# Optimization experiments

Measured on AMD Instinct MI355X. Metric: run time of the kernel, lower is better.

## Reference

```python
import jax, jax.numpy as jnp
import numpy as np

B, NQ, NK, D, H = 4, 512, 512, 128, 32  # batch, n_queries, n_keys, kq_size, mlp hidden


def setup_inputs() -> dict:
    key = jax.random.key(0)
    ks = jax.random.split(key, 7)
    s_in = 1.0 / np.sqrt(2 * D)
    s_h = 1.0 / np.sqrt(H)
    return {
        "keys": jax.random.normal(ks[0], (B, NK, D), dtype=jnp.float32),
        "queries": jax.random.normal(ks[1], (B, NQ, D), dtype=jnp.float32),
        # first MLP layer Linear(2D, H) split into key-half and query-half
        "Wk": jax.random.uniform(ks[2], (D, H), jnp.float32, -s_in, s_in),
        "Wq": jax.random.uniform(ks[3], (D, H), jnp.float32, -s_in, s_in),
        "b1": jax.random.uniform(ks[4], (H,), jnp.float32, -s_in, s_in),
        # second MLP layer Linear(H, 1)
        "w2": jax.random.uniform(ks[5], (H,), jnp.float32, -s_h, s_h),
        "b2": jax.random.uniform(ks[6], (), jnp.float32, -s_h, s_h),
    }


def reference(keys, queries, Wk, Wq, b1, w2, b2):
    # AdditiveScorer: logits[b,q,k] = w2 . tanh(W1 @ [keys[b,k]; queries[b,q]] + b1) + b2
    # Split the concat-linear into two GEMMs (identical math, no [B,Q,K,2D] tensor).
    kh = jnp.einsum("bkd,dh->bkh", keys, Wk)            # (B, NK, H)
    qh = jnp.einsum("bqd,dh->bqh", queries, Wq)          # (B, NQ, H)
    h = jnp.tanh(qh[:, :, None, :] + kh[:, None, :, :] + b1)  # (B, NQ, NK, H)
    logits = jnp.einsum("bqkh,h->bqk", h, w2) + b2       # (B, NQ, NK)
    attn = jax.nn.softmax(logits, axis=-1)               # softmax over keys
    context = jnp.einsum("bqk,bkd->bqd", attn, keys)     # weighted value sum (values = keys)
    return context
```

## Files before the change

### kernel.cpp

```cpp
#include <hip/hip_runtime.h>

#define B 4
#define NQ 512
#define NK 512
#define D 128
#define H 32
#define G 4
#define PS 2.8853900817779268f

__device__ __forceinline__ float rcp_f(float x)  { return __builtin_amdgcn_rcpf(x); }
__device__ __forceinline__ float exp2_f(float x) { return __builtin_amdgcn_exp2f(x); }

__device__ __forceinline__ void fma4(float4& a, const float4& v, float s) {
    a.x = fmaf(s, v.x, a.x);
    a.y = fmaf(s, v.y, a.y);
    a.z = fmaf(s, v.z, a.z);
    a.w = fmaf(s, v.w, a.w);
}

__global__ __launch_bounds__(256) void proj_kernel(
    const float* __restrict__ keys, const float* __restrict__ queries,
    const float* __restrict__ Wk, const float* __restrict__ Wq,
    const float* __restrict__ b1,
    float* __restrict__ Ek, float* __restrict__ eq)
{
    __shared__ float xs[8][D];
    const int tid = threadIdx.x;
    const int r0 = blockIdx.x * 8;
    const bool is_q = (r0 >= B * NK);
    const float* __restrict__ X = is_q ? (queries + (size_t)(r0 - B * NK) * D)
                                       : (keys + (size_t)r0 * D);
    const float* __restrict__ W = is_q ? Wq : Wk;

    reinterpret_cast<float4*>(&xs[0][0])[tid] =
        reinterpret_cast<const float4*>(X)[tid];
    __syncthreads();

    const int lr = tid >> 5;
    const int h  = tid & 31;
    float a0 = 0.f, a1 = 0.f, a2 = 0.f, a3 = 0.f;
    const float4* x4 = reinterpret_cast<const float4*>(&xs[lr][0]);
    #pragma unroll
    for (int i = 0; i < D / 4; ++i) {
        float4 v = x4[i];
        a0 = fmaf(v.x, W[(4 * i + 0) * H + h], a0);
        a1 = fmaf(v.y, W[(4 * i + 1) * H + h], a1);
        a2 = fmaf(v.z, W[(4 * i + 2) * H + h], a2);
        a3 = fmaf(v.w, W[(4 * i + 3) * H + h], a3);
    }
    float acc = (a0 + a1) + (a2 + a3);
    if (is_q) {
        const int rq = r0 - B * NK + lr;
        eq[(size_t)rq * H + h] = exp2_f(acc * PS);
    } else {
        const int r = r0 + lr;
        const int b = r >> 9;
        const int k = r & (NK - 1);
        Ek[((size_t)b * H + h) * NK + k] = exp2_f((acc + b1[h]) * PS);
    }
}

__global__ __launch_bounds__(512, 4) void attend_kernel(
    const float* __restrict__ keys,
    const float* __restrict__ Ek,
    const float* __restrict__ eq,
    const float* __restrict__ w2,
    float* __restrict__ outp)
{
    __shared__ float exw[NK][G];
    __shared__ float accm[16][G][D];
    float* red = &accm[0][0][0];

    const int tid = threadIdx.x;
    const int b   = blockIdx.x >> 7;
    const int q0  = (blockIdx.x & 127) * G;

    const float* Ekc = Ek + (size_t)b * H * NK + tid;
    float ek[H];
    #pragma unroll
    for (int h = 0; h < H; ++h) ek[h] = Ekc[h * NK];

    const float* eqb = eq + ((size_t)b * NQ + q0) * H;
    float acc[G];
    #pragma unroll
    for (int g = 0; g < G; ++g) acc[g] = 0.f;

    #pragma unroll
    for (int h4 = 0; h4 < H; h4 += 4) {
        const float w0 = w2[h4 + 0];
        const float w1 = w2[h4 + 1];
        const float wc = w2[h4 + 2];
        const float w3 = w2[h4 + 3];
        #pragma unroll
        for (int g = 0; g < G; ++g) {
            const float d0 = fmaf(eqb[g * H + h4 + 0], ek[h4 + 0], 1.f);
            const float d1 = fmaf(eqb[g * H + h4 + 1], ek[h4 + 1], 1.f);
            const float d2 = fmaf(eqb[g * H + h4 + 2], ek[h4 + 2], 1.f);
            const float d3 = fmaf(eqb[g * H + h4 + 3], ek[h4 + 3], 1.f);
            const float nab = fmaf(w1, d0, w0 * d1);
            const float ncd = fmaf(w3, d2, wc * d3);
            const float dab = d0 * d1;
            const float dcd = d2 * d3;
            const float n4  = fmaf(nab, dcd, ncd * dab);
            const float d4  = dab * dcd;
            acc[g] = fmaf(n4, rcp_f(d4), acc[g]);
        }
    }
    float e0 = exp2_f(-PS * acc[0]);
    float e1 = exp2_f(-PS * acc[1]);
    float e2 = exp2_f(-PS * acc[2]);
    float e3 = exp2_f(-PS * acc[3]);

    float s0 = e0, s1 = e1, s2 = e2, s3 = e3;
    #pragma unroll
    for (int off = 32; off; off >>= 1) {
        s0 += __shfl_xor(s0, off);
        s1 += __shfl_xor(s1, off);
        s2 += __shfl_xor(s2, off);
        s3 += __shfl_xor(s3, off);
    }
    if ((tid & 63) == 0)
        *reinterpret_cast<float4*>(red + (tid >> 6) * G) = float4{s0, s1, s2, s3};
    __syncthreads();
    float4 sum = {0.f, 0.f, 0.f, 0.f};
    #pragma unroll
    for (int p = 0; p < 8; ++p) {
        const float4 v = *reinterpret_cast<const float4*>(red + p * G);
        sum.x += v.x; sum.y += v.y; sum.z += v.z; sum.w += v.w;
    }
    *reinterpret_cast<float4*>(&exw[tid][0]) =
        float4{e0 * rcp_f(sum.x), e1 * rcp_f(sum.y),
               e2 * rcp_f(sum.z), e3 * rcp_f(sum.w)};
    __syncthreads();

    const int dg = tid & 31;
    const int kp = tid >> 5;
    const float4* k4 = reinterpret_cast<const float4*>(
        keys + ((size_t)b * NK + kp * 32) * D) + dg;
    float4 a0 = {0,0,0,0}, a1 = a0, a2 = a0, a3 = a0;

    float4 kbA[8], kbB[8];
    #pragma unroll
    for (int j = 0; j < 8; ++j) kbA[j] = k4[(size_t)j * (D / 4)];
    #pragma unroll
    for (int c = 0; c < 4; ++c) {
        float4* cur = (c & 1) ? kbB : kbA;
        float4* nxt = (c & 1) ? kbA : kbB;
        if (c < 3) {
            #pragma unroll
            for (int j = 0; j < 8; ++j)
                nxt[j] = k4[(size_t)((c + 1) * 8 + j) * (D / 4)];
        }
        #pragma unroll
        for (int j = 0; j < 8; ++j) {
            const int kk = c * 8 + j;
            const float4 ev = *reinterpret_cast<const float4*>(&exw[kp * 32 + kk][0]);
            fma4(a0, cur[j], ev.x);
            fma4(a1, cur[j], ev.y);
            fma4(a2, cur[j], ev.z);
            fma4(a3, cur[j], ev.w);
        }
    }
    *reinterpret_cast<float4*>(&accm[kp][0][4 * dg]) = a0;
    *reinterpret_cast<float4*>(&accm[kp][1][4 * dg]) = a1;
    *reinterpret_cast<float4*>(&accm[kp][2][4 * dg]) = a2;
    *reinterpret_cast<float4*>(&accm[kp][3][4 * dg]) = a3;
    __syncthreads();

    const int g = tid >> 7;
    const int d = tid & 127;
    float r = 0.f;
    #pragma unroll
    for (int p = 0; p < 16; ++p) r += accm[p][g][d];
    outp[((size_t)b * NQ + q0 + g) * D + d] = r;
}

extern "C" void kernel_launch(void* const* d_in, const int* in_sizes, int n_in,
                              void* d_out, int out_size, void* d_ws, size_t ws_size,
                              hipStream_t stream) {
    const float* keys    = (const float*)d_in[0];
    const float* queries = (const float*)d_in[1];
    const float* Wk      = (const float*)d_in[2];
    const float* Wq      = (const float*)d_in[3];
    const float* b1      = (const float*)d_in[4];
    const float* w2      = (const float*)d_in[5];
    float* out = (float*)d_out;

    float* Ek = (float*)d_ws;
    float* eq = Ek + (size_t)B * H * NK;

    const int proj_blocks = (B * NK + B * NQ) / 8;
    proj_kernel<<<proj_blocks, 256, 0, stream>>>(keys, queries, Wk, Wq, b1, Ek, eq);
    attend_kernel<<<B * NQ / G, 512, 0, stream>>>(keys, Ek, eq, w2, out);
}
```

Baseline: 20.10 us.

## Compute attention-weighted key sum with split-bf16 MFMA instead of fp32 FMAs

The proj kernel now also writes the keys transposed as high/low bf16 pairs. The attend kernel stores the softmax weights as hi/lo bf16 in shared memory and computes the context with three 16x16x32 bf16 MFMAs per k-step, which approximates fp32 precision. This drops the fp32 FMA loop and the 16-way shared-memory partial reduction. The cost is extra workspace traffic, bf16 split work, and a small precision loss from dropping the lo*lo term. Only a quarter of the lanes write output, since the MFMA result is replicated across them.

Result: slower. 30.92 us (+53.8%).

```diff
diff --git a/kernel.cpp b/kernel.cpp
--- a/kernel.cpp
+++ b/kernel.cpp
@@ -7,22 +7,27 @@
 #define H 32
 #define G 4
 #define PS 2.8853900817779268f
+#define NKP (NK + 8)
+
+typedef float f32x4 __attribute__((ext_vector_type(4)));
+typedef short bf16x8 __attribute__((ext_vector_type(8)));
 
 __device__ __forceinline__ float rcp_f(float x)  { return __builtin_amdgcn_rcpf(x); }
 __device__ __forceinline__ float exp2_f(float x) { return __builtin_amdgcn_exp2f(x); }
 
-__device__ __forceinline__ void fma4(float4& a, const float4& v, float s) {
-    a.x = fmaf(s, v.x, a.x);
-    a.y = fmaf(s, v.y, a.y);
-    a.z = fmaf(s, v.z, a.z);
-    a.w = fmaf(s, v.w, a.w);
+__device__ __forceinline__ void bf16_split(float x, unsigned short& h, unsigned short& l) {
+    unsigned bits = __float_as_uint(x);
+    h = (unsigned short)(bits >> 16);
+    float hf = __uint_as_float((unsigned)h << 16);
+    l = (unsigned short)(__float_as_uint(x - hf) >> 16);
 }
 
 __global__ __launch_bounds__(256) void proj_kernel(
     const float* __restrict__ keys, const float* __restrict__ queries,
     const float* __restrict__ Wk, const float* __restrict__ Wq,
     const float* __restrict__ b1,
-    float* __restrict__ Ek, float* __restrict__ eq)
+    float* __restrict__ Ek, float* __restrict__ eq,
+    unsigned short* __restrict__ khi, unsigned short* __restrict__ klo)
 {
     __shared__ float xs[8][D];
     const int tid = threadIdx.x;
@@ -58,18 +63,34 @@
         const int k = r & (NK - 1);
         Ek[((size_t)b * H + h) * NK + k] = exp2_f((acc + b1[h]) * PS);
     }
+
+    if (!is_q) {
+        const int bb = r0 >> 9;
+        const int k0 = r0 & (NK - 1);
+        const int d  = tid >> 1;
+        const int kq = (tid & 1) * 4;
+        ushort4 h4, l4;
+        unsigned short* hp = reinterpret_cast<unsigned short*>(&h4);
+        unsigned short* lp = reinterpret_cast<unsigned short*>(&l4);
+        #pragma unroll
+        for (int j = 0; j < 4; ++j)
+            bf16_split(xs[kq + j][d], hp[j], lp[j]);
+        *reinterpret_cast<ushort4*>(&khi[((size_t)bb * D + d) * NK + k0 + kq]) = h4;
+        *reinterpret_cast<ushort4*>(&klo[((size_t)bb * D + d) * NK + k0 + kq]) = l4;
+    }
 }
 
 __global__ __launch_bounds__(512, 4) void attend_kernel(
-    const float* __restrict__ keys,
+    const unsigned short* __restrict__ khi,
+    const unsigned short* __restrict__ klo,
     const float* __restrict__ Ek,
     const float* __restrict__ eq,
     const float* __restrict__ w2,
     float* __restrict__ outp)
 {
-    __shared__ float exw[NK][G];
-    __shared__ float accm[16][G][D];
-    float* red = &accm[0][0][0];
+    __shared__ unsigned short ex_hi[G][NKP];
+    __shared__ unsigned short ex_lo[G][NKP];
+    __shared__ float red[8][G];
 
     const int tid = threadIdx.x;
     const int b   = blockIdx.x >> 7;
@@ -102,8 +123,7 @@
             const float dab = d0 * d1;
             const float dcd = d2 * d3;
             const float n4  = fmaf(nab, dcd, ncd * dab);
-            const float d4  = dab * dcd;
-            acc[g] = fmaf(n4, rcp_f(d4), acc[g]);
+            acc[g] = fmaf(n4, rcp_f(dab * dcd), acc[g]);
         }
     }
     float e0 = exp2_f(-PS * acc[0]);
@@ -120,59 +140,51 @@
         s3 += __shfl_xor(s3, off);
     }
     if ((tid & 63) == 0)
-        *reinterpret_cast<float4*>(red + (tid >> 6) * G) = float4{s0, s1, s2, s3};
+        *reinterpret_cast<float4*>(&red[tid >> 6][0]) = float4{s0, s1, s2, s3};
     __syncthreads();
     float4 sum = {0.f, 0.f, 0.f, 0.f};
     #pragma unroll
     for (int p = 0; p < 8; ++p) {
-        const float4 v = *reinterpret_cast<const float4*>(red + p * G);
+        const float4 v = *reinterpret_cast<const float4*>(&red[p][0]);
         sum.x += v.x; sum.y += v.y; sum.z += v.z; sum.w += v.w;
     }
-    *reinterpret_cast<float4*>(&exw[tid][0]) =
-        float4{e0 * rcp_f(sum.x), e1 * rcp_f(sum.y),
-               e2 * rcp_f(sum.z), e3 * rcp_f(sum.w)};
+    {
+        const float v0 = e0 * rcp_f(sum.x);
+        const float v1 = e1 * rcp_f(sum.y);
+        const float v2 = e2 * rcp_f(sum.z);
+        const float v3 = e3 * rcp_f(sum.w);
+        unsigned short h, l;
+        bf16_split(v0, h, l); ex_hi[0][tid] = h; ex_lo[0][tid] = l;
+        bf16_split(v1, h, l); ex_hi[1][tid] = h; ex_lo[1][tid] = l;
+        bf16_split(v2, h, l); ex_hi[2][tid] = h; ex_lo[2][tid] = l;
+        bf16_split(v3, h, l); ex_hi[3][tid] = h; ex_lo[3][tid] = l;
+    }
     __syncthreads();
 
-    const int dg = tid & 31;
-    const int kp = tid >> 5;
-    const float4* k4 = reinterpret_cast<const float4*>(
-        keys + ((size_t)b * NK + kp * 32) * D) + dg;
-    float4 a0 = {0,0,0,0}, a1 = a0, a2 = a0, a3 = a0;
-
-    float4 kbA[8], kbB[8];
-    #pragma unroll
-    for (int j = 0; j < 8; ++j) kbA[j] = k4[(size_t)j * (D / 4)];
-    #pragma unroll
-    for (int c = 0; c < 4; ++c) {
-        float4* cur = (c & 1) ? kbB : kbA;
-        float4* nxt = (c & 1) ? kbA : kbB;
-        if (c < 3) {
-            #pragma unroll
-            for (int j = 0; j < 8; ++j)
-                nxt[j] = k4[(size_t)((c + 1) * 8 + j) * (D / 4)];
-        }
+    const int lane = tid & 63;
+    const int w    = tid >> 6;
+    const int kgrp = lane >> 4;
+    const int dcol = w * 16 + (lane & 15);
+    const unsigned short* bh_base = khi + ((size_t)b * D + dcol) * NK;
+    const unsigned short* bl_base = klo + ((size_t)b * D + dcol) * NK;
+
+    f32x4 c = {0.f, 0.f, 0.f, 0.f};
+    #pragma unroll 4
+    for (int s = 0; s < 16; ++s) {
+        const int ko = s * 32 + kgrp * 8;
+        const bf16x8 ah = *reinterpret_cast<const bf16x8*>(&ex_hi[lane & 3][ko]);
+        const bf16x8 al = *reinterpret_cast<const bf16x8*>(&ex_lo[lane & 3][ko]);
+        const bf16x8 bh = *reinterpret_cast<const bf16x8*>(bh_base + ko);
+        const bf16x8 bl = *reinterpret_cast<const bf16x8*>(bl_base + ko);
+        c = __builtin_amdgcn_mfma_f32_16x16x32_bf16(ah, bh, c, 0, 0, 0);
+        c = __builtin_amdgcn_mfma_f32_16x16x32_bf16(al, bh, c, 0, 0, 0);
+        c = __builtin_amdgcn_mfma_f32_16x16x32_bf16(ah, bl, c, 0, 0, 0);
+    }
+    if (kgrp == 0) {
         #pragma unroll
-        for (int j = 0; j < 8; ++j) {
-            const int kk = c * 8 + j;
-            const float4 ev = *reinterpret_cast<const float4*>(&exw[kp * 32 + kk][0]);
-            fma4(a0, cur[j], ev.x);
-            fma4(a1, cur[j], ev.y);
-            fma4(a2, cur[j], ev.z);
-            fma4(a3, cur[j], ev.w);
-        }
-    }
-    *reinterpret_cast<float4*>(&accm[kp][0][4 * dg]) = a0;
-    *reinterpret_cast<float4*>(&accm[kp][1][4 * dg]) = a1;
-    *reinterpret_cast<float4*>(&accm[kp][2][4 * dg]) = a2;
-    *reinterpret_cast<float4*>(&accm[kp][3][4 * dg]) = a3;
-    __syncthreads();
-
-    const int g = tid >> 7;
-    const int d = tid & 127;
-    float r = 0.f;
-    #pragma unroll
-    for (int p = 0; p < 16; ++p) r += accm[p][g][d];
-    outp[((size_t)b * NQ + q0 + g) * D + d] = r;
+        for (int r = 0; r < 4; ++r)
+            outp[((size_t)b * NQ + q0 + r) * D + dcol] = c[r];
+    }
 }
 
 extern "C" void kernel_launch(void* const* d_in, const int* in_sizes, int n_in,
@@ -188,8 +200,11 @@
 
     float* Ek = (float*)d_ws;
     float* eq = Ek + (size_t)B * H * NK;
+    unsigned short* khi = (unsigned short*)(eq + (size_t)B * NQ * H);
+    unsigned short* klo = khi + (size_t)B * D * NK;
 
     const int proj_blocks = (B * NK + B * NQ) / 8;
-    proj_kernel<<<proj_blocks, 256, 0, stream>>>(keys, queries, Wk, Wq, b1, Ek, eq);
-    attend_kernel<<<B * NQ / G, 512, 0, stream>>>(keys, Ek, eq, w2, out);
-}
+    proj_kernel<<<proj_blocks, 256, 0, stream>>>(keys, queries, Wk, Wq, b1,
+                                                 Ek, eq, khi, klo);
+    attend_kernel<<<B * NQ / G, 512, 0, stream>>>(khi, klo, Ek, eq, w2, out);
+}
```
